# Kernel tuning notes

Hardware: AMD Instinct MI355X
Metric: run time of the kernel (lower is better)

## Reference

```python
import jax, jax.numpy as jnp
import numpy as np

EPS = 1e-8  # torch F.cosine_similarity eps


def setup_inputs() -> dict:
    key = jax.random.key(0)
    k1, k2, k3 = jax.random.split(key, 3)
    bn, cn, dim = 4096, 8192, 1024
    x = jax.random.normal(k1, (bn, dim), dtype=jnp.float32)
    positive = jax.random.normal(k2, (bn, dim), dtype=jnp.float32)
    negative = jax.random.normal(k3, (cn, dim), dtype=jnp.float32)
    return {"x": x, "positive": positive, "negative": negative}


def reference(x, positive, negative):
    bn = x.shape[0]
    nx = jnp.linalg.norm(x, axis=1)          # (bn,)
    npos = jnp.linalg.norm(positive, axis=1)  # (bn,)
    nneg = jnp.linalg.norm(negative, axis=1)  # (cn,)
    # positive cosine similarity, torch-style eps clamp on norm product
    sim = jnp.sum(x * positive, axis=1) / jnp.maximum(nx * npos, EPS)  # (bn,)
    # negative cosine similarities via one matmul instead of (bn,cn,dim) repeats
    neg_sim = (x @ negative.T) / jnp.maximum(nx[:, None] * nneg[None, :], EPS)  # (bn,cn)
    p = jnp.exp(sim) / jnp.sum(jnp.exp(neg_sim), axis=1)  # (bn,)
    loss = -jnp.sum(jnp.log(p)) / bn
    return loss
```

## Files before the change

### kernel.cpp

```cpp
#include <hip/hip_runtime.h>
#include <stdint.h>
#include <stddef.h>

#define DIM 1024
#define EPS 1e-8f

typedef __attribute__((ext_vector_type(4)))  int   i32x4;
typedef __attribute__((ext_vector_type(8)))  int   i32x8;
typedef __attribute__((ext_vector_type(4)))  float f32x4;

#define SCALE8 0x7B7B7B7B

__device__ __forceinline__ void async_copy16(const void* g, void* l) {
    __builtin_amdgcn_global_load_lds(
        (__attribute__((address_space(1))) void*)const_cast<void*>(g),
        (__attribute__((address_space(3))) void*)(l), 16, 0, 0);
}

__global__ __launch_bounds__(256)
void prep_all(const float* __restrict__ x, const float* __restrict__ pos,
              const float* __restrict__ neg,
              unsigned char* __restrict__ Xn, unsigned char* __restrict__ Nn,
              float* __restrict__ simOut, float* __restrict__ rowsum, int bn) {
    const int lane = threadIdx.x & 63;
    const int wave = threadIdx.x >> 6;
    const int grow = blockIdx.x * 4 + wave;
    const bool isX = grow < bn;
    const int row  = isX ? grow : grow - bn;
    const float* src = isX ? x : neg;
    unsigned char* dst = isX ? Xn : Nn;

    const float4* s = (const float4*)(src + (size_t)row * DIM);
    float4 xv[4], pv[4];
    float sxx = 0.f, spp = 0.f, sxp = 0.f;
#pragma unroll
    for (int i = 0; i < 4; i++) {
        xv[i] = s[lane + 64 * i];
        sxx += xv[i].x * xv[i].x + xv[i].y * xv[i].y + xv[i].z * xv[i].z + xv[i].w * xv[i].w;
    }
    if (isX) {
        const float4* p = (const float4*)(pos + (size_t)row * DIM);
#pragma unroll
        for (int i = 0; i < 4; i++) {
            pv[i] = p[lane + 64 * i];
            spp += pv[i].x * pv[i].x + pv[i].y * pv[i].y + pv[i].z * pv[i].z + pv[i].w * pv[i].w;
            sxp += xv[i].x * pv[i].x + xv[i].y * pv[i].y + xv[i].z * pv[i].z + xv[i].w * pv[i].w;
        }
#pragma unroll
        for (int off = 1; off < 64; off <<= 1) {
            sxx += __shfl_xor(sxx, off);
            spp += __shfl_xor(spp, off);
            sxp += __shfl_xor(sxp, off);
        }
    } else {
#pragma unroll
        for (int off = 1; off < 64; off <<= 1) sxx += __shfl_xor(sxx, off);
    }
    const float nx  = sqrtf(sxx);
    const float inv = (nx > 0.f) ? (16.f / nx) : 0.f;
    if (isX && lane == 0) {
        const float np = sqrtf(spp);
        simOut[row] = sxp / fmaxf(nx * np, EPS);
        rowsum[row] = 0.f;
    }
    unsigned int t;
    t = __builtin_amdgcn_cvt_pk_fp8_f32(xv[0].x * inv, xv[0].y * inv, 0, false);
    unsigned int q0 = __builtin_amdgcn_cvt_pk_fp8_f32(xv[0].z * inv, xv[0].w * inv, t, true);
    t = __builtin_amdgcn_cvt_pk_fp8_f32(xv[1].x * inv, xv[1].y * inv, 0, false);
    unsigned int q1 = __builtin_amdgcn_cvt_pk_fp8_f32(xv[1].z * inv, xv[1].w * inv, t, true);
    t = __builtin_amdgcn_cvt_pk_fp8_f32(xv[2].x * inv, xv[2].y * inv, 0, false);
    unsigned int q2 = __builtin_amdgcn_cvt_pk_fp8_f32(xv[2].z * inv, xv[2].w * inv, t, true);
    t = __builtin_amdgcn_cvt_pk_fp8_f32(xv[3].x * inv, xv[3].y * inv, 0, false);
    unsigned int q3 = __builtin_amdgcn_cvt_pk_fp8_f32(xv[3].z * inv, xv[3].w * inv, t, true);

    unsigned int* wr = (unsigned int*)(dst + (size_t)row * DIM);
    wr[lane]       = q0;
    wr[lane + 64]  = q1;
    wr[lane + 128] = q2;
    wr[lane + 192] = q3;
}

__global__ __launch_bounds__(256, 3)
void gemm_exp_rowsum(const unsigned char* __restrict__ Xn,
                     const unsigned char* __restrict__ Nn,
                     float* __restrict__ rowsum) {
    constexpr int KB = DIM;
    constexpr int BK = 128;
    __shared__ __align__(16) unsigned char Ash[128 * BK];
    __shared__ __align__(16) unsigned char Bsh[128 * BK];

    const int tid  = threadIdx.x;
    const int lane = tid & 63;
    const int wave = tid >> 6;
    const int rowBase = blockIdx.y * 128;
    const int colBase = blockIdx.x * 128;

    const int srow = lane >> 3;
    const int sch  = (lane & 7) ^ srow;
    const int w32  = wave * 32;
    const unsigned char* gA = Xn + (size_t)(rowBase + w32 + srow) * KB + sch * 16;
    const unsigned char* gB = Nn + (size_t)(colBase + w32 + srow) * KB + sch * 16;

    const f32x4 fz = {0.f, 0.f, 0.f, 0.f};
    f32x4 acc[4][4];
#pragma unroll
    for (int mi = 0; mi < 4; mi++)
#pragma unroll
        for (int ni = 0; ni < 4; ni++) acc[mi][ni] = fz;

    const int m0   = (wave >> 1) * 64;
    const int n0   = (wave & 1) * 64;
    const int mrow = lane & 15;
    const int q    = lane >> 4;
    const int c0   = ((2 * q) ^ (mrow & 7)) << 4;

    int aoff[4], boff[4];
#pragma unroll
    for (int i = 0; i < 4; i++) {
        aoff[i] = (m0 + 16 * i + mrow) * BK + c0;
        boff[i] = (n0 + 16 * i + mrow) * BK + c0;
    }

#define STAGE(stg)                                                        \
    do {                                                                  \
        const int kq = (stg) * BK;                                        \
        _Pragma("unroll")                                                 \
        for (int i = 0; i < 4; i++) {                                     \
            async_copy16(gA + (size_t)(8 * i) * KB + kq, Ash + (w32 + 8 * i) * BK); \
            async_copy16(gB + (size_t)(8 * i) * KB + kq, Bsh + (w32 + 8 * i) * BK); \
        }                                                                 \
    } while (0)

#define COMPUTE()                                                         \
    do {                                                                  \
        i32x8 Af[4], Bf[4];                                               \
        _Pragma("unroll")                                                 \
        for (int i = 0; i < 4; i++) {                                     \
            i32x4 alo = *(const i32x4*)(Ash + aoff[i]);                   \
            i32x4 ahi = *(const i32x4*)(Ash + (aoff[i] ^ 16));            \
            Af[i] = __builtin_shufflevector(alo, ahi, 0, 1, 2, 3, 4, 5, 6, 7); \
            i32x4 blo = *(const i32x4*)(Bsh + boff[i]);                   \
            i32x4 bhi = *(const i32x4*)(Bsh + (boff[i] ^ 16));            \
            Bf[i] = __builtin_shufflevector(blo, bhi, 0, 1, 2, 3, 4, 5, 6, 7); \
        }                                                                 \
        _Pragma("unroll")                                                 \
        for (int mi = 0; mi < 4; mi++)                                    \
            _Pragma("unroll")                                             \
            for (int ni = 0; ni < 4; ni++)                                \
                acc[mi][ni] = __builtin_amdgcn_mfma_scale_f32_16x16x128_f8f6f4( \
                    Af[mi], Bf[ni], acc[mi][ni], 0, 0, 0, SCALE8, 0, SCALE8); \
    } while (0)

#pragma unroll
    for (int s = 0; s < 8; s++) {
        STAGE(s);
        asm volatile("s_waitcnt vmcnt(0)\n\ts_barrier" ::: "memory");
        COMPUTE();
        __syncthreads();
    }
#undef STAGE
#undef COMPUTE

#pragma unroll
    for (int mi = 0; mi < 4; mi++) {
        float rs0 = 0.f, rs1 = 0.f, rs2 = 0.f, rs3 = 0.f;
#pragma unroll
        for (int ni = 0; ni < 4; ni++) {
            rs0 += __expf(acc[mi][ni].x);
            rs1 += __expf(acc[mi][ni].y);
            rs2 += __expf(acc[mi][ni].z);
            rs3 += __expf(acc[mi][ni].w);
        }
#pragma unroll
        for (int off = 1; off < 16; off <<= 1) {
            rs0 += __shfl_xor(rs0, off);
            rs1 += __shfl_xor(rs1, off);
            rs2 += __shfl_xor(rs2, off);
            rs3 += __shfl_xor(rs3, off);
        }
        if ((lane & 15) == 0) {
            const int r = rowBase + m0 + mi * 16 + q * 4;
            atomicAdd(&rowsum[r + 0], rs0);
            atomicAdd(&rowsum[r + 1], rs1);
            atomicAdd(&rowsum[r + 2], rs2);
            atomicAdd(&rowsum[r + 3], rs3);
        }
    }
}

__global__ __launch_bounds__(1024)
void loss_kernel(const float* __restrict__ rowsum, const float* __restrict__ sim,
                 float* __restrict__ out, int bn) {
    const int tid  = threadIdx.x;
    const int lane = tid & 63;
    const int wave = tid >> 6;
    float acc = 0.f;
    for (int i = tid; i < bn; i += 1024) acc += logf(rowsum[i]) - sim[i];
#pragma unroll
    for (int off = 1; off < 64; off <<= 1) acc += __shfl_xor(acc, off);
    __shared__ float red[16];
    if (lane == 0) red[wave] = acc;
    __syncthreads();
    if (tid == 0) {
        float t = 0.f;
#pragma unroll
        for (int i = 0; i < 16; i++) t += red[i];
        out[0] = t / (float)bn;
    }
}

extern "C" void kernel_launch(void* const* d_in, const int* in_sizes, int n_in,
                              void* d_out, int out_size, void* d_ws, size_t ws_size,
                              hipStream_t stream) {
    const float* x   = (const float*)d_in[0];
    const float* pos = (const float*)d_in[1];
    const float* neg = (const float*)d_in[2];
    const int bn = in_sizes[0] / DIM;
    const int cn = in_sizes[2] / DIM;

    unsigned char* Xn = (unsigned char*)d_ws;
    unsigned char* Nn = Xn + (size_t)bn * DIM;
    float* sim    = (float*)(Nn + (size_t)cn * DIM);
    float* rowsum = sim + bn;

    prep_all<<<dim3((bn + cn) / 4), dim3(256), 0, stream>>>(x, pos, neg, Xn, Nn, sim, rowsum, bn);
    gemm_exp_rowsum<<<dim3(cn / 128, bn / 128), dim3(256), 0, stream>>>(Xn, Nn, rowsum);
    loss_kernel<<<dim3(1), dim3(1024), 0, stream>>>(rowsum, sim, (float*)d_out, bn);
}
```

Before: 169.2 us.

## Triple-buffer fp8 GEMM with 256x128 tiles, 8 waves and grid swizzle

The fused fp8 GEMM+exp+rowsum kernel moves from a single-buffered 128x128 tile with 4 waves to a 256x128 tile with 8 waves and a three-stage LDS ring in dynamic shared memory (144 KB). Each K step is split into two halves so global-to-LDS async copies for stage k+2 overlap MFMA work on stage k. MFMA issue is raised in priority with s_setprio, and workgroup IDs are swizzled for L2 locality. The cost is larger LDS use, which limits occupancy, and a more intricate waitcnt/barrier schedule that must stay correct.

```diff
diff --git a/kernel.cpp b/kernel.cpp
--- a/kernel.cpp
+++ b/kernel.cpp
@@ -80,26 +80,30 @@
     wr[lane + 192] = q3;
 }
 
-__global__ __launch_bounds__(256, 3)
+__global__ __launch_bounds__(512, 2)
 void gemm_exp_rowsum(const unsigned char* __restrict__ Xn,
                      const unsigned char* __restrict__ Nn,
                      float* __restrict__ rowsum) {
-    constexpr int KB = DIM;
-    constexpr int BK = 128;
-    __shared__ __align__(16) unsigned char Ash[128 * BK];
-    __shared__ __align__(16) unsigned char Bsh[128 * BK];
+    constexpr int KB   = DIM;
+    constexpr int BK   = 128;
+    constexpr int BUFB = 256 * BK + 128 * BK;
+    constexpr int BOFF = 256 * BK;
+    extern __shared__ unsigned char smem[];
 
     const int tid  = threadIdx.x;
     const int lane = tid & 63;
     const int wave = tid >> 6;
-    const int rowBase = blockIdx.y * 128;
-    const int colBase = blockIdx.x * 128;
+
+    const int nwg  = gridDim.x * gridDim.y;
+    const int bid  = blockIdx.y * gridDim.x + blockIdx.x;
+    const int swz  = (bid & 7) * (nwg >> 3) + (bid >> 3);
+    const int rowBase = (swz / gridDim.x) * 256;
+    const int colBase = (swz % gridDim.x) * 128;
 
     const int srow = lane >> 3;
     const int sch  = (lane & 7) ^ srow;
-    const int w32  = wave * 32;
-    const unsigned char* gA = Xn + (size_t)(rowBase + w32 + srow) * KB + sch * 16;
-    const unsigned char* gB = Nn + (size_t)(colBase + w32 + srow) * KB + sch * 16;
+    const unsigned char* gA = Xn + (size_t)(rowBase + wave * 32 + srow) * KB + sch * 16;
+    const unsigned char* gB = Nn + (size_t)(colBase + wave * 16 + srow) * KB + sch * 16;
 
     const f32x4 fz = {0.f, 0.f, 0.f, 0.f};
     f32x4 acc[4][4];
@@ -118,48 +122,73 @@
 #pragma unroll
     for (int i = 0; i < 4; i++) {
         aoff[i] = (m0 + 16 * i + mrow) * BK + c0;
-        boff[i] = (n0 + 16 * i + mrow) * BK + c0;
-    }
-
-#define STAGE(stg)                                                        \
-    do {                                                                  \
-        const int kq = (stg) * BK;                                        \
-        _Pragma("unroll")                                                 \
-        for (int i = 0; i < 4; i++) {                                     \
-            async_copy16(gA + (size_t)(8 * i) * KB + kq, Ash + (w32 + 8 * i) * BK); \
-            async_copy16(gB + (size_t)(8 * i) * KB + kq, Bsh + (w32 + 8 * i) * BK); \
-        }                                                                 \
+        boff[i] = BOFF + (n0 + 16 * i + mrow) * BK + c0;
+    }
+
+#define STAGE_HALF(buf, stg, h)                                                \
+    do {                                                                       \
+        const int kq = (stg) * BK;                                             \
+        unsigned char* Lb = smem + (buf) * BUFB;                               \
+        async_copy16(gA + (size_t)(16 * (h)) * KB + kq,                        \
+                     Lb + (wave * 32 + 16 * (h)) * BK);                        \
+        async_copy16(gA + (size_t)(16 * (h) + 8) * KB + kq,                    \
+                     Lb + (wave * 32 + 16 * (h) + 8) * BK);                    \
+        async_copy16(gB + (size_t)(8 * (h)) * KB + kq,                         \
+                     Lb + BOFF + (wave * 16 + 8 * (h)) * BK);                  \
     } while (0)
 
-#define COMPUTE()                                                         \
-    do {                                                                  \
-        i32x8 Af[4], Bf[4];                                               \
-        _Pragma("unroll")                                                 \
-        for (int i = 0; i < 4; i++) {                                     \
-            i32x4 alo = *(const i32x4*)(Ash + aoff[i]);                   \
-            i32x4 ahi = *(const i32x4*)(Ash + (aoff[i] ^ 16));            \
-            Af[i] = __builtin_shufflevector(alo, ahi, 0, 1, 2, 3, 4, 5, 6, 7); \
-            i32x4 blo = *(const i32x4*)(Bsh + boff[i]);                   \
-            i32x4 bhi = *(const i32x4*)(Bsh + (boff[i] ^ 16));            \
-            Bf[i] = __builtin_shufflevector(blo, bhi, 0, 1, 2, 3, 4, 5, 6, 7); \
-        }                                                                 \
-        _Pragma("unroll")                                                 \
-        for (int mi = 0; mi < 4; mi++)                                    \
-            _Pragma("unroll")                                             \
-            for (int ni = 0; ni < 4; ni++)                                \
-                acc[mi][ni] = __builtin_amdgcn_mfma_scale_f32_16x16x128_f8f6f4( \
-                    Af[mi], Bf[ni], acc[mi][ni], 0, 0, 0, SCALE8, 0, SCALE8); \
+#define RD(base, off, dst)                                                     \
+    do {                                                                       \
+        i32x4 lo_ = *(const i32x4*)((base) + (off));                           \
+        i32x4 hi_ = *(const i32x4*)((base) + ((off) ^ 16));                    \
+        dst = __builtin_shufflevector(lo_, hi_, 0, 1, 2, 3, 4, 5, 6, 7);       \
     } while (0)
 
-#pragma unroll
-    for (int s = 0; s < 8; s++) {
-        STAGE(s);
-        asm volatile("s_waitcnt vmcnt(0)\n\ts_barrier" ::: "memory");
-        COMPUTE();
-        __syncthreads();
-    }
-#undef STAGE
-#undef COMPUTE
+    STAGE_HALF(0, 0, 0);
+    STAGE_HALF(0, 0, 1);
+    STAGE_HALF(1, 1, 0);
+    STAGE_HALF(1, 1, 1);
+    asm volatile("s_waitcnt vmcnt(6)\n\ts_barrier" ::: "memory");
+
+#pragma unroll
+    for (int w = 0; w < 8; w++) {
+        const int b  = w % 3;
+        const int nb = (w + 2) % 3;
+        const unsigned char* Ab = smem + b * BUFB;
+        i32x8 Af[4], Bf[2];
+        if (w < 6) STAGE_HALF(nb, w + 2, 0);
+#pragma unroll
+        for (int i = 0; i < 4; i++) RD(Ab, aoff[i], Af[i]);
+#pragma unroll
+        for (int i = 0; i < 2; i++) RD(Ab, boff[i], Bf[i]);
+        __builtin_amdgcn_s_setprio(1);
+#pragma unroll
+        for (int mi = 0; mi < 4; mi++)
+#pragma unroll
+            for (int ni = 0; ni < 2; ni++)
+                acc[mi][ni] = __builtin_amdgcn_mfma_scale_f32_16x16x128_f8f6f4(
+                    Af[mi], Bf[ni], acc[mi][ni], 0, 0, 0, SCALE8, 0, SCALE8);
+        __builtin_amdgcn_s_setprio(0);
+        asm volatile("s_barrier" ::: "memory");
+        if (w < 6) STAGE_HALF(nb, w + 2, 1);
+#pragma unroll
+        for (int i = 0; i < 2; i++) RD(Ab, boff[2 + i], Bf[i]);
+        __builtin_amdgcn_s_setprio(1);
+#pragma unroll
+        for (int mi = 0; mi < 4; mi++)
+#pragma unroll
+            for (int ni = 0; ni < 2; ni++)
+                acc[mi][2 + ni] = __builtin_amdgcn_mfma_scale_f32_16x16x128_f8f6f4(
+                    Af[mi], Bf[ni], acc[mi][2 + ni], 0, 0, 0, SCALE8, 0, SCALE8);
+        __builtin_amdgcn_s_setprio(0);
+        if (w < 6) {
+            asm volatile("s_waitcnt vmcnt(6)\n\ts_barrier" ::: "memory");
+        } else if (w == 6) {
+            asm volatile("s_waitcnt vmcnt(0)\n\ts_barrier" ::: "memory");
+        }
+    }
+#undef STAGE_HALF
+#undef RD
 
 #pragma unroll
     for (int mi = 0; mi < 4; mi++) {
@@ -223,7 +252,15 @@
     float* sim    = (float*)(Nn + (size_t)cn * DIM);
     float* rowsum = sim + bn;
 
+    static bool attr_done = false;
+    if (!attr_done) {
+        (void)hipFuncSetAttribute((const void*)gemm_exp_rowsum,
+                                  hipFuncAttributeMaxDynamicSharedMemorySize,
+                                  147456);
+        attr_done = true;
+    }
+
     prep_all<<<dim3((bn + cn) / 4), dim3(256), 0, stream>>>(x, pos, neg, Xn, Nn, sim, rowsum, bn);
-    gemm_exp_rowsum<<<dim3(cn / 128, bn / 128), dim3(256), 0, stream>>>(Xn, Nn, rowsum);
+    gemm_exp_rowsum<<<dim3(cn / 128, bn / 256), dim3(512), 147456, stream>>>(Xn, Nn, rowsum);
     loss_kernel<<<dim3(1), dim3(1024), 0, stream>>>(rowsum, sim, (float*)d_out, bn);
 }
```

Result: faster. 157.0 us (-7.2%).
